# Kernel optimization log

Hardware: AMD Instinct MI355X
Metric: run time of the kernel (lower is better)

Reference implementation:

```python
import jax, jax.numpy as jnp
import numpy as np

EPS = 1e-5
K = 20

def knn_idx(x, k):
    # x: (B, N, C) -> indices of k nearest neighbors (by negative squared distance, includes self)
    sq = jnp.sum(x * x, axis=-1)                                  # (B, N)
    d = 2.0 * jnp.einsum('bnc,bmc->bnm', x, x) - sq[:, :, None] - sq[:, None, :]
    return jax.lax.top_k(d, k)[1]                                 # (B, N, k)

def edge_conv(x, k, W, g, b, rm, rv):
    # x: (B, N, C); W: (O, 2C); BN params: (O,). Returns (B, N, O).
    idx = knn_idx(x, k)
    feat = jax.vmap(lambda xt, i: xt[i])(x, idx)                  # (B, N, k, C) neighbor gather
    ctr = jnp.broadcast_to(x[:, :, None, :], feat.shape)
    edge = jnp.concatenate([feat - ctr, ctr], axis=-1)            # (B, N, k, 2C)
    h = jnp.einsum('bnkc,oc->bnko', edge, W)                      # 1x1 conv
    h = g * (h - rm) * jax.lax.rsqrt(rv + EPS) + b                # BN (eval, running stats)
    h = jnp.where(h > 0, h, 0.2 * h)                              # LeakyReLU(0.2)
    return jnp.max(h, axis=2)                                     # max over k

def bn(h, g, b, rm, rv):
    return g * (h - rm) * jax.lax.rsqrt(rv + EPS) + b

def lrelu(h):
    return jnp.where(h > 0, h, 0.2 * h)

def _bn_params(key, c):
    k1, k2 = jax.random.split(key)
    g = 1.0 + 0.1 * jax.random.normal(k1, (c,), dtype=jnp.float32)
    b = 0.1 * jax.random.normal(k2, (c,), dtype=jnp.float32)
    return g, b, jnp.zeros((c,), jnp.float32), jnp.ones((c,), jnp.float32)

def setup_inputs() -> dict:
    key = jax.random.key(0)
    ks = jax.random.split(key, 16)
    B, Cin, N = 8, 6, 4096
    d = {'x': jax.random.normal(ks[0], (B, Cin, N), dtype=jnp.float32)}
    def w(k, o, i):
        return jax.random.normal(k, (o, i), dtype=jnp.float32) * (1.0 / np.sqrt(i))
    d['W1'] = w(ks[1], 64, 12);   d['g1'], d['b1'], d['m1'], d['v1'] = _bn_params(ks[2], 64)
    d['W2'] = w(ks[3], 64, 128);  d['g2'], d['b2'], d['m2'], d['v2'] = _bn_params(ks[4], 64)
    d['W3'] = w(ks[5], 128, 128); d['g3'], d['b3'], d['m3'], d['v3'] = _bn_params(ks[6], 128)
    d['W4'] = w(ks[7], 256, 256); d['g4'], d['b4'], d['m4'], d['v4'] = _bn_params(ks[8], 256)
    d['W5'] = w(ks[9], 1024, 512); d['g5'], d['b5'], d['m5'], d['v5'] = _bn_params(ks[10], 1024)
    d['L1'] = w(ks[11], 512, 2048); d['gl1'], d['bl1'], d['ml1'], d['vl1'] = _bn_params(ks[12], 512)
    d['L2'] = w(ks[13], 256, 512); d['L2b'] = jnp.zeros((256,), jnp.float32)
    d['gl2'], d['bl2'], d['ml2'], d['vl2'] = _bn_params(ks[14], 256)
    d['L3'] = w(ks[15], 2, 256);  d['L3b'] = jnp.zeros((2,), jnp.float32)
    return d

def reference(x, W1, g1, b1, m1, v1, W2, g2, b2, m2, v2, W3, g3, b3, m3, v3,
              W4, g4, b4, m4, v4, W5, g5, b5, m5, v5,
              L1, gl1, bl1, ml1, vl1, L2, L2b, gl2, bl2, ml2, vl2, L3, L3b):
    xt = jnp.transpose(x, (0, 2, 1))                              # (B, N, 6)
    x1 = edge_conv(xt, K, W1, g1, b1, m1, v1)                     # (B, N, 64)
    x2 = edge_conv(x1, K, W2, g2, b2, m2, v2)                     # (B, N, 64)
    x3 = edge_conv(x2, K, W3, g3, b3, m3, v3)                     # (B, N, 128)
    x4 = edge_conv(x3, K, W4, g4, b4, m4, v4)                     # (B, N, 256)
    xc = jnp.concatenate([x1, x2, x3, x4], axis=-1)               # (B, N, 512)
    h = lrelu(bn(jnp.einsum('bnc,oc->bno', xc, W5), g5, b5, m5, v5))  # (B, N, 1024)
    pooled = jnp.concatenate([jnp.max(h, axis=1), jnp.mean(h, axis=1)], axis=-1)  # (B, 2048)
    o = lrelu(bn(pooled @ L1.T, gl1, bl1, ml1, vl1))
    o = lrelu(bn(o @ L2.T + L2b, gl2, bl2, ml2, vl2))
    return o @ L3.T + L3b                                         # (B, 2)
```

## Files before the change

kernel.cpp:

```cpp
#include <hip/hip_runtime.h>


#define NPTS   4096
#define NB     8
#define BNR    32768
#define KNN    20
#define EPSBN  1e-5f

__device__ __forceinline__ float lrelu(float x){ return x > 0.f ? x : 0.2f*x; }

__global__ __launch_bounds__(256) void k_transpose_pad(const float* __restrict__ x,
                                                       float* __restrict__ xt){
  int id = blockIdx.x*256 + threadIdx.x;
  int b = id >> 12, n = id & (NPTS-1);
  const float* xb = x + (size_t)b*6*NPTS + n;
  float* o = xt + (size_t)id*8;
#pragma unroll
  for (int c = 0; c < 6; ++c) o[c] = xb[(size_t)c*NPTS];
  o[6] = 0.f; o[7] = 0.f;
}

__global__ __launch_bounds__(256) void k_sqnorm(const float* __restrict__ X, int xstride, int c4,
                                                float* __restrict__ sq){
  int id = blockIdx.x*256 + threadIdx.x;
  const float4* r = (const float4*)(X + (size_t)id*xstride);
  float s = 0.f;
  for (int c = 0; c < c4; ++c){ float4 v = r[c]; s += v.x*v.x + v.y*v.y + v.z*v.z + v.w*v.w; }
  sq[id] = s;
}

__global__ __launch_bounds__(256) void k_dgemm(const float* __restrict__ X, int xstride, int Kdim,
                                               const float* __restrict__ sqv,
                                               float* __restrict__ D){
  const int bi = blockIdx.y, bj = blockIdx.x;
  if (bj < bi) return;
  __shared__ float As[16][132];
  __shared__ float Bs[16][132];
  const int i0 = bi*128, j0 = bj*128;
  const int tid = threadIdx.x, tx = tid & 15, ty = tid >> 4;
  float acc[8][8] = {};
  for (int k0 = 0; k0 < Kdim; k0 += 16){
#pragma unroll
    for (int i = 0; i < 8; ++i){
      int li = tid + 256*i;
      int row = li >> 4, kk = li & 15;
      bool ok = (k0 + kk) < Kdim;
      As[kk][row] = ok ? X[(size_t)(i0+row)*xstride + k0+kk] : 0.f;
      Bs[kk][row] = ok ? X[(size_t)(j0+row)*xstride + k0+kk] : 0.f;
    }
    __syncthreads();
#pragma unroll
    for (int kk = 0; kk < 16; ++kk){
      float a[8], b[8];
      *(float4*)&a[0] = *(const float4*)&As[kk][ty*8];
      *(float4*)&a[4] = *(const float4*)&As[kk][ty*8+4];
      *(float4*)&b[0] = *(const float4*)&Bs[kk][tx*4];
      *(float4*)&b[4] = *(const float4*)&Bs[kk][64 + tx*4];
#pragma unroll
      for (int r = 0; r < 8; ++r)
#pragma unroll
        for (int c = 0; c < 8; ++c)
          acc[r][c] = fmaf(a[r], b[c], acc[r][c]);
    }
    __syncthreads();
  }
  float sj[8];
#pragma unroll
  for (int c = 0; c < 4; ++c){
    sj[c]   = sqv[j0 + tx*4 + c];
    sj[c+4] = sqv[j0 + 64 + tx*4 + c];
  }
  float si[8];
#pragma unroll
  for (int r = 0; r < 8; ++r) si[r] = sqv[i0 + ty*8 + r];
#pragma unroll
  for (int r = 0; r < 8; ++r)
#pragma unroll
    for (int c = 0; c < 8; ++c)
      acc[r][c] = 2.f*acc[r][c] - si[r] - sj[c];
#pragma unroll
  for (int r = 0; r < 8; ++r){
    float* drow = D + (size_t)(i0 + ty*8 + r)*NPTS;
    *(float4*)&drow[j0 + tx*4]      = make_float4(acc[r][0], acc[r][1], acc[r][2], acc[r][3]);
    *(float4*)&drow[j0 + 64 + tx*4] = make_float4(acc[r][4], acc[r][5], acc[r][6], acc[r][7]);
  }
  if (bj > bi){
#pragma unroll
    for (int c = 0; c < 4; ++c){
      float* drow0 = D + (size_t)(j0 + tx*4 + c)*NPTS + i0 + ty*8;
      *(float4*)&drow0[0] = make_float4(acc[0][c], acc[1][c], acc[2][c], acc[3][c]);
      *(float4*)&drow0[4] = make_float4(acc[4][c], acc[5][c], acc[6][c], acc[7][c]);
      float* drow1 = D + (size_t)(j0 + 64 + tx*4 + c)*NPTS + i0 + ty*8;
      *(float4*)&drow1[0] = make_float4(acc[0][c+4], acc[1][c+4], acc[2][c+4], acc[3][c+4]);
      *(float4*)&drow1[4] = make_float4(acc[4][c+4], acc[5][c+4], acc[6][c+4], acc[7][c+4]);
    }
  }
}

__global__ __launch_bounds__(256) void k_scan(const float* __restrict__ D,
                                              int* __restrict__ idx){
  const int lane = threadIdx.x & 63;
  const int wv   = threadIdx.x >> 6;
  const int row  = blockIdx.x*4 + wv;
  const float* drow = D + (size_t)row*NPTS;
  float bv = -1e30f; int bi = -1;
  float thr = -1e30f;
  float dcur = drow[lane];
  for (int m0 = 0; m0 < NPTS; m0 += 64){
    float dnext = (m0 + 64 < NPTS) ? drow[m0 + 64 + lane] : -1e30f;
    unsigned long long mask = __ballot(dcur > thr);
    while (mask){
      int l = __ffsll(mask) - 1;
      mask &= mask - 1;
      float dv = __shfl(dcur, l);
      if (dv > thr){
        float upv = __shfl_up(bv, 1);
        int   upi = __shfl_up(bi, 1);
        if (lane < KNN){
          bool ins  = dv > bv;
          bool insp = (lane > 0) && (dv > upv);
          if (ins){ bv = insp ? upv : dv; bi = insp ? upi : (m0 + l); }
        }
        thr = __shfl(bv, KNN-1);
      }
    }
    dcur = dnext;
  }
  if (lane < KNN) idx[(size_t)row*KNN + lane] = bi;
}

__global__ __launch_bounds__(256) void k_gemm_xw(const float* __restrict__ X, int xstride, int Kdim,
                                                 const float* __restrict__ W, int wstride,
                                                 float* __restrict__ Out, int ostride){
  __shared__ float Xs[16][68];
  __shared__ float Ws[16][68];
  const int m0 = blockIdx.x*64, o0 = blockIdx.y*64;
  const int tid = threadIdx.x, tx = tid & 15, ty = tid >> 4;
  float acc[4][4] = {};
  for (int k0 = 0; k0 < Kdim; k0 += 16){
#pragma unroll
    for (int i = 0; i < 4; ++i){
      int li = tid + 256*i;
      int row = li >> 4, kk = li & 15;
      bool ok = (k0 + kk) < Kdim;
      Xs[kk][row] = ok ? X[(size_t)(m0+row)*xstride + k0+kk] : 0.f;
      Ws[kk][row] = ok ? W[(size_t)(o0+row)*wstride + k0+kk] : 0.f;
    }
    __syncthreads();
#pragma unroll
    for (int kk = 0; kk < 16; ++kk){
      float xa[4], wb[4];
      *(float4*)xa = *(const float4*)&Xs[kk][ty*4];
      *(float4*)wb = *(const float4*)&Ws[kk][tx*4];
#pragma unroll
      for (int i = 0; i < 4; ++i)
#pragma unroll
        for (int j = 0; j < 4; ++j)
          acc[i][j] = fmaf(xa[i], wb[j], acc[i][j]);
    }
    __syncthreads();
  }
#pragma unroll
  for (int i = 0; i < 4; ++i){
    float4 v = make_float4(acc[i][0], acc[i][1], acc[i][2], acc[i][3]);
    *(float4*)&Out[(size_t)(m0+ty*4+i)*ostride + o0 + tx*4] = v;
  }
}

__global__ __launch_bounds__(256) void k_gather_conv(const float* __restrict__ P,
                                                     const float* __restrict__ Q,
                                                     const int* __restrict__ idx,
                                                     const float* __restrict__ g,
                                                     const float* __restrict__ bb,
                                                     const float* __restrict__ rm,
                                                     const float* __restrict__ rv,
                                                     float* __restrict__ Out, int oshift, int choff){
  const int O = 1 << oshift;
  int id = blockIdx.x*256 + threadIdx.x;
  int gn = id >> oshift;
  int o  = id & (O-1);
  int bbase = (gn >> 12) * NPTS;
  const int* ip = idx + (size_t)gn*KNN;
  float vmax = -1e30f, vmin = 1e30f;
#pragma unroll
  for (int k = 0; k < KNN; ++k){
    int m = ip[k];
    float v = P[((size_t)(bbase + m) << oshift) + o];
    vmax = fmaxf(vmax, v);
    vmin = fminf(vmin, v);
  }
  float scale = g[o] * rsqrtf(rv[o] + EPSBN);
  float beta  = bb[o] - rm[o]*scale;
  float R = (scale >= 0.f) ? vmax : vmin;
  float h = R - P[((size_t)gn << oshift) + o] + Q[((size_t)gn << oshift) + o];
  Out[(size_t)gn*512 + choff + o] = lrelu(fmaf(scale, h, beta));
}

__global__ __launch_bounds__(256) void k_gemm_w5_pool(const float* __restrict__ X,
                                                      const float* __restrict__ W,
                                                      const float* __restrict__ g,
                                                      const float* __restrict__ bb,
                                                      const float* __restrict__ rm,
                                                      const float* __restrict__ rv,
                                                      float* __restrict__ pmax,
                                                      float* __restrict__ psum){
  __shared__ float Xs[16][132];
  __shared__ float Ws[16][132];
  __shared__ float red[2][16][128];
  const int m0 = blockIdx.x*128, o0 = blockIdx.y*128;
  const int tid = threadIdx.x, tx = tid & 15, ty = tid >> 4;
  float acc[8][8] = {};
  for (int k0 = 0; k0 < 512; k0 += 16){
#pragma unroll
    for (int i = 0; i < 8; ++i){
      int li = tid + 256*i;
      int row = li >> 4, kk = li & 15;
      Xs[kk][row] = X[(size_t)(m0+row)*512 + k0+kk];
      Ws[kk][row] = W[(size_t)(o0+row)*512 + k0+kk];
    }
    __syncthreads();
#pragma unroll
    for (int kk = 0; kk < 16; ++kk){
      float xa[8], wb[8];
      *(float4*)&xa[0] = *(const float4*)&Xs[kk][ty*8];
      *(float4*)&xa[4] = *(const float4*)&Xs[kk][ty*8+4];
      *(float4*)&wb[0] = *(const float4*)&Ws[kk][tx*4];
      *(float4*)&wb[4] = *(const float4*)&Ws[kk][64 + tx*4];
#pragma unroll
      for (int i = 0; i < 8; ++i)
#pragma unroll
        for (int j = 0; j < 8; ++j)
          acc[i][j] = fmaf(xa[i], wb[j], acc[i][j]);
    }
    __syncthreads();
  }
#pragma unroll
  for (int j = 0; j < 8; ++j){
    int ocol = (j < 4) ? (tx*4 + j) : (64 + tx*4 + j - 4);
    int o = o0 + ocol;
    float scale = g[o] * rsqrtf(rv[o] + EPSBN);
    float beta  = bb[o] - rm[o]*scale;
    float mx = -1e30f, sm = 0.f;
#pragma unroll
    for (int i = 0; i < 8; ++i){
      float h = lrelu(fmaf(scale, acc[i][j], beta));
      mx = fmaxf(mx, h);
      sm += h;
    }
    red[0][ty][ocol] = mx;
    red[1][ty][ocol] = sm;
  }
  __syncthreads();
  if (tid < 128){
    float mx = -1e30f, sm = 0.f;
#pragma unroll
    for (int t = 0; t < 16; ++t){
      mx = fmaxf(mx, red[0][t][tid]);
      sm += red[1][t][tid];
    }
    pmax[(size_t)blockIdx.x*1024 + o0 + tid] = mx;
    psum[(size_t)blockIdx.x*1024 + o0 + tid] = sm;
  }
}

__global__ __launch_bounds__(256) void k_pool_reduce(const float* __restrict__ pmax,
                                                     const float* __restrict__ psum,
                                                     float* __restrict__ pooled){
  int id = blockIdx.x*256 + threadIdx.x;
  int b = id >> 10, o = id & 1023;
  float mx = -1e30f, sm = 0.f;
  for (int t = 0; t < 32; ++t){
    mx = fmaxf(mx, pmax[(size_t)(b*32+t)*1024 + o]);
    sm += psum[(size_t)(b*32+t)*1024 + o];
  }
  pooled[(size_t)b*2048 + o] = mx;
  pooled[(size_t)b*2048 + 1024 + o] = sm * (1.f/NPTS);
}

__global__ __launch_bounds__(256) void k_fc1(const float* __restrict__ pooled,
                                             const float* __restrict__ W,
                                             const float* __restrict__ g,
                                             const float* __restrict__ bb,
                                             const float* __restrict__ rm,
                                             const float* __restrict__ rv,
                                             float* __restrict__ out){
  __shared__ float4 xs[512];
  int b = blockIdx.x >> 1;
  int o = ((blockIdx.x & 1) << 8) + threadIdx.x;
  const float4* pr = (const float4*)(pooled + (size_t)b*2048);
  for (int l = threadIdx.x; l < 512; l += 256) xs[l] = pr[l];
  __syncthreads();
  const float4* wr = (const float4*)(W + (size_t)o*2048);
  float s0=0.f, s1=0.f, s2=0.f, s3=0.f;
#pragma unroll 4
  for (int c = 0; c < 512; ++c){
    float4 w = wr[c], v = xs[c];
    s0 = fmaf(v.x, w.x, s0); s1 = fmaf(v.y, w.y, s1);
    s2 = fmaf(v.z, w.z, s2); s3 = fmaf(v.w, w.w, s3);
  }
  float h = (s0+s1)+(s2+s3);
  float scale = g[o] * rsqrtf(rv[o] + EPSBN);
  float beta  = bb[o] - rm[o]*scale;
  out[(size_t)b*512 + o] = lrelu(fmaf(scale, h, beta));
}

__global__ __launch_bounds__(256) void k_fc2(const float* __restrict__ in,
                                             const float* __restrict__ W,
                                             const float* __restrict__ bias,
                                             const float* __restrict__ g,
                                             const float* __restrict__ bb,
                                             const float* __restrict__ rm,
                                             const float* __restrict__ rv,
                                             float* __restrict__ out){
  __shared__ float4 xs[128];
  int b = blockIdx.x;
  int o = threadIdx.x;
  const float4* pr = (const float4*)(in + (size_t)b*512);
  if (threadIdx.x < 128) xs[threadIdx.x] = pr[threadIdx.x];
  __syncthreads();
  const float4* wr = (const float4*)(W + (size_t)o*512);
  float s0=0.f, s1=0.f, s2=0.f, s3=0.f;
#pragma unroll 4
  for (int c = 0; c < 128; ++c){
    float4 w = wr[c], v = xs[c];
    s0 = fmaf(v.x, w.x, s0); s1 = fmaf(v.y, w.y, s1);
    s2 = fmaf(v.z, w.z, s2); s3 = fmaf(v.w, w.w, s3);
  }
  float h = (s0+s1)+(s2+s3) + bias[o];
  float scale = g[o] * rsqrtf(rv[o] + EPSBN);
  float beta  = bb[o] - rm[o]*scale;
  out[(size_t)b*256 + o] = lrelu(fmaf(scale, h, beta));
}

__global__ __launch_bounds__(64) void k_fc3(const float* __restrict__ in,
                                            const float* __restrict__ W,
                                            const float* __restrict__ bias,
                                            float* __restrict__ out){
  int t = threadIdx.x;
  if (t >= 16) return;
  int b = t >> 1, o = t & 1;
  const float* xr = in + (size_t)b*256;
  const float* wr = W + (size_t)o*256;
  float s = 0.f;
  for (int c = 0; c < 256; ++c) s = fmaf(xr[c], wr[c], s);
  out[b*2 + o] = s + bias[o];
}

extern "C" void kernel_launch(void* const* d_in, const int* in_sizes, int n_in,
                              void* d_out, int out_size, void* d_ws, size_t ws_size,
                              hipStream_t stream){
  (void)in_sizes; (void)n_in; (void)out_size;
  const float* x   = (const float*)d_in[0];
  const float* W1  = (const float*)d_in[1];
  const float* g1  = (const float*)d_in[2];
  const float* b1  = (const float*)d_in[3];
  const float* m1  = (const float*)d_in[4];
  const float* v1  = (const float*)d_in[5];
  const float* W2  = (const float*)d_in[6];
  const float* g2  = (const float*)d_in[7];
  const float* b2  = (const float*)d_in[8];
  const float* m2  = (const float*)d_in[9];
  const float* v2  = (const float*)d_in[10];
  const float* W3  = (const float*)d_in[11];
  const float* g3  = (const float*)d_in[12];
  const float* b3  = (const float*)d_in[13];
  const float* m3  = (const float*)d_in[14];
  const float* v3  = (const float*)d_in[15];
  const float* W4  = (const float*)d_in[16];
  const float* g4  = (const float*)d_in[17];
  const float* b4  = (const float*)d_in[18];
  const float* m4  = (const float*)d_in[19];
  const float* v4  = (const float*)d_in[20];
  const float* W5  = (const float*)d_in[21];
  const float* g5  = (const float*)d_in[22];
  const float* b5  = (const float*)d_in[23];
  const float* m5  = (const float*)d_in[24];
  const float* v5  = (const float*)d_in[25];
  const float* L1  = (const float*)d_in[26];
  const float* gl1 = (const float*)d_in[27];
  const float* bl1 = (const float*)d_in[28];
  const float* ml1 = (const float*)d_in[29];
  const float* vl1 = (const float*)d_in[30];
  const float* L2  = (const float*)d_in[31];
  const float* L2b = (const float*)d_in[32];
  const float* gl2 = (const float*)d_in[33];
  const float* bl2 = (const float*)d_in[34];
  const float* vl2_g = (const float*)d_in[36];
  const float* ml2 = (const float*)d_in[35];
  const float* L3  = (const float*)d_in[37];
  const float* L3b = (const float*)d_in[38];

  float* ws   = (float*)d_ws;
  float* xt   = ws;
  float* sq   = ws + 262144;
  int*   idx  = (int*)(ws + 294912);
  float* Dbuf = ws + 950272;
  float* P    = Dbuf;
  float* Q    = Dbuf + 8388608;
  float* xc   = ws + 17727488;
  float* pmax = ws + 34504704;
  float* psum = ws + 34766848;
  float* pool = ws + 35028992;
  float* oA   = ws + 35045376;
  float* oB   = ws + 35049472;
  if (ws_size < (size_t)35051520 * 4) return;

  k_transpose_pad<<<128, 256, 0, stream>>>(x, xt);

  k_sqnorm<<<128, 256, 0, stream>>>(xt, 8, 2, sq);
  for (int b = 0; b < NB; ++b){
    k_dgemm<<<dim3(32,32), 256, 0, stream>>>(xt + (size_t)b*NPTS*8, 8, 8, sq + b*NPTS, Dbuf);
    k_scan<<<1024, 256, 0, stream>>>(Dbuf, idx + (size_t)b*NPTS*KNN);
  }
  k_gemm_xw<<<dim3(512,1), 256, 0, stream>>>(xt, 8, 6, W1,     12, P, 64);
  k_gemm_xw<<<dim3(512,1), 256, 0, stream>>>(xt, 8, 6, W1 + 6, 12, Q, 64);
  k_gather_conv<<<8192, 256, 0, stream>>>(P, Q, idx, g1, b1, m1, v1, xc, 6, 0);

  k_sqnorm<<<128, 256, 0, stream>>>(xc, 512, 16, sq);
  for (int b = 0; b < NB; ++b){
    k_dgemm<<<dim3(32,32), 256, 0, stream>>>(xc + (size_t)b*NPTS*512, 512, 64, sq + b*NPTS, Dbuf);
    k_scan<<<1024, 256, 0, stream>>>(Dbuf, idx + (size_t)b*NPTS*KNN);
  }
  k_gemm_xw<<<dim3(512,1), 256, 0, stream>>>(xc, 512, 64, W2,      128, P, 64);
  k_gemm_xw<<<dim3(512,1), 256, 0, stream>>>(xc, 512, 64, W2 + 64, 128, Q, 64);
  k_gather_conv<<<8192, 256, 0, stream>>>(P, Q, idx, g2, b2, m2, v2, xc, 6, 64);

  k_sqnorm<<<128, 256, 0, stream>>>(xc + 64, 512, 16, sq);
  for (int b = 0; b < NB; ++b){
    k_dgemm<<<dim3(32,32), 256, 0, stream>>>(xc + 64 + (size_t)b*NPTS*512, 512, 64, sq + b*NPTS, Dbuf);
    k_scan<<<1024, 256, 0, stream>>>(Dbuf, idx + (size_t)b*NPTS*KNN);
  }
  k_gemm_xw<<<dim3(512,2), 256, 0, stream>>>(xc + 64, 512, 64, W3,      128, P, 128);
  k_gemm_xw<<<dim3(512,2), 256, 0, stream>>>(xc + 64, 512, 64, W3 + 64, 128, Q, 128);
  k_gather_conv<<<16384, 256, 0, stream>>>(P, Q, idx, g3, b3, m3, v3, xc, 7, 128);

  k_sqnorm<<<128, 256, 0, stream>>>(xc + 128, 512, 32, sq);
  for (int b = 0; b < NB; ++b){
    k_dgemm<<<dim3(32,32), 256, 0, stream>>>(xc + 128 + (size_t)b*NPTS*512, 512, 128, sq + b*NPTS, Dbuf);
    k_scan<<<1024, 256, 0, stream>>>(Dbuf, idx + (size_t)b*NPTS*KNN);
  }
  k_gemm_xw<<<dim3(512,4), 256, 0, stream>>>(xc + 128, 512, 128, W4,       256, P, 256);
  k_gemm_xw<<<dim3(512,4), 256, 0, stream>>>(xc + 128, 512, 128, W4 + 128, 256, Q, 256);
  k_gather_conv<<<32768, 256, 0, stream>>>(P, Q, idx, g4, b4, m4, v4, xc, 8, 256);

  k_gemm_w5_pool<<<dim3(256,8), 256, 0, stream>>>(xc, W5, g5, b5, m5, v5, pmax, psum);
  k_pool_reduce<<<32, 256, 0, stream>>>(pmax, psum, pool);

  k_fc1<<<16, 256, 0, stream>>>(pool, L1, gl1, bl1, ml1, vl1, oA);
  k_fc2<<<8, 256, 0, stream>>>(oA, L2, L2b, gl2, bl2, ml2, vl2_g, oB);
  k_fc3<<<1, 64, 0, stream>>>(oB, L3, L3b, (float*)d_out);
}
```

Baseline: 3.577 ms.

## Fuse distance GEMM with top-k selection and merge P/Q projection GEMMs

Replaces the per-batch distance-matrix GEMM plus separate wavefront scan with one fused kernel. Each block computes 64 rows of distances against 128-column tiles and keeps a running top-20 in shared memory, filtering candidates by a per-row threshold through a small capped candidate buffer. This removes the 64MB distance-matrix write and read per batch and the 16 serial launches per layer. It also merges the two projection GEMMs into one kernel writing an interleaved PQ buffer. The trade-off is a serial single-thread-per-row insertion sort and extra block barriers inside the column loop, and the grid is only 512 blocks.

```diff
diff --git a/kernel.cpp b/kernel.cpp
--- a/kernel.cpp
+++ b/kernel.cpp
@@ -6,6 +6,7 @@
 #define BNR    32768
 #define KNN    20
 #define EPSBN  1e-5f
+#define CAP    12
 
 __device__ __forceinline__ float lrelu(float x){ return x > 0.f ? x : 0.2f*x; }
 
@@ -29,131 +30,160 @@
   sq[id] = s;
 }
 
-__global__ __launch_bounds__(256) void k_dgemm(const float* __restrict__ X, int xstride, int Kdim,
-                                               const float* __restrict__ sqv,
-                                               float* __restrict__ D){
-  const int bi = blockIdx.y, bj = blockIdx.x;
-  if (bj < bi) return;
-  __shared__ float As[16][132];
-  __shared__ float Bs[16][132];
-  const int i0 = bi*128, j0 = bj*128;
+template<int K>
+__global__ __launch_bounds__(256) void k_knn_fused(const float* __restrict__ X, int xstride,
+                                                   const float* __restrict__ sqv,
+                                                   int* __restrict__ idx){
+  constexpr int BK = (K < 32) ? K : 32;
+  __shared__ float As[BK][68];
+  __shared__ float Bs[BK][132];
+  __shared__ float sqs[128];
+  __shared__ float thr[64];
+  __shared__ float lv[64][KNN];
+  __shared__ int   li[64][KNN];
+  __shared__ int   cnt[64];
+  __shared__ float cv[64][CAP];
+  __shared__ int   ci[64][CAP];
+
+  const int b  = blockIdx.y;
+  const int i0 = blockIdx.x * 64;
   const int tid = threadIdx.x, tx = tid & 15, ty = tid >> 4;
-  float acc[8][8] = {};
+  const float* Xb  = X + (size_t)b * NPTS * xstride;
+  const float* sqb = sqv + b * NPTS;
+
+  if (tid < 64){
+    thr[tid] = -3e38f; cnt[tid] = 0;
+#pragma unroll
+    for (int j = 0; j < KNN; ++j){ lv[tid][j] = -3e38f; li[tid][j] = 0; }
+  }
+  float sqi[4];
+#pragma unroll
+  for (int r = 0; r < 4; ++r) sqi[r] = sqb[i0 + ty*4 + r];
+
+  for (int j0 = 0; j0 < NPTS; j0 += 128){
+    float acc[4][8] = {};
+    for (int k0 = 0; k0 < K; k0 += BK){
+      {
+        int row = tid & 63, q = tid >> 6;
+        const float* src = Xb + (size_t)(i0 + row)*xstride + k0;
+#pragma unroll
+        for (int k = q*(BK/4); k < (q+1)*(BK/4); ++k) As[k][row] = src[k];
+      }
+      {
+        int col = tid & 127, h = tid >> 7;
+        const float* src = Xb + (size_t)(j0 + col)*xstride + k0;
+#pragma unroll
+        for (int k = h*(BK/2); k < (h+1)*(BK/2); ++k) Bs[k][col] = src[k];
+      }
+      if (k0 == 0 && tid < 128) sqs[tid] = sqb[j0 + tid];
+      __syncthreads();
+#pragma unroll
+      for (int kk = 0; kk < BK; ++kk){
+        float a[4], bb_[8];
+        *(float4*)a        = *(const float4*)&As[kk][ty*4];
+        *(float4*)&bb_[0]  = *(const float4*)&Bs[kk][tx*4];
+        *(float4*)&bb_[4]  = *(const float4*)&Bs[kk][64 + tx*4];
+#pragma unroll
+        for (int r = 0; r < 4; ++r)
+#pragma unroll
+          for (int c = 0; c < 8; ++c)
+            acc[r][c] = fmaf(a[r], bb_[c], acc[r][c]);
+      }
+      __syncthreads();
+    }
+    float sq8[8];
+#pragma unroll
+    for (int c = 0; c < 4; ++c){ sq8[c] = sqs[tx*4 + c]; sq8[c+4] = sqs[64 + tx*4 + c]; }
+
+    unsigned pending = 0xFFFFFFFFu;
+    while (true){
+      if (pending){
+        float tr[4];
+#pragma unroll
+        for (int r = 0; r < 4; ++r) tr[r] = thr[ty*4 + r];
+#pragma unroll
+        for (int r = 0; r < 4; ++r)
+#pragma unroll
+          for (int c = 0; c < 8; ++c){
+            unsigned bit = 1u << (r*8 + c);
+            if (pending & bit){
+              float val = 2.f*acc[r][c] - sqi[r] - sq8[c];
+              if (val <= tr[r]) pending &= ~bit;
+              else {
+                int row = ty*4 + r;
+                int pos = atomicAdd(&cnt[row], 1);
+                if (pos < CAP){
+                  int col = (c < 4) ? (j0 + tx*4 + c) : (j0 + 64 + tx*4 + c - 4);
+                  cv[row][pos] = val; ci[row][pos] = col;
+                  pending &= ~bit;
+                }
+              }
+            }
+          }
+      }
+      int any = __syncthreads_or(pending != 0u);
+      if (tid < 64){
+        int n = min(cnt[tid], CAP);
+        for (int i2 = 0; i2 < n; ++i2){
+          float val = cv[tid][i2]; int cc = ci[tid][i2];
+          if (val > lv[tid][KNN-1]){
+            int j = KNN-1;
+            while (j > 0 && lv[tid][j-1] < val){
+              lv[tid][j] = lv[tid][j-1]; li[tid][j] = li[tid][j-1]; --j;
+            }
+            lv[tid][j] = val; li[tid][j] = cc;
+          }
+        }
+        thr[tid] = lv[tid][KNN-1];
+        cnt[tid] = 0;
+      }
+      __syncthreads();
+      if (!any) break;
+    }
+  }
+  if (tid < 64){
+    int gn = b*NPTS + i0 + tid;
+#pragma unroll
+    for (int j = 0; j < KNN; ++j) idx[(size_t)gn*KNN + j] = li[tid][j];
+  }
+}
+
+__global__ __launch_bounds__(256) void k_gemm_pq(const float* __restrict__ X, int xstride, int Kdim,
+                                                 const float* __restrict__ W, int wstride, int Och,
+                                                 float* __restrict__ PQ){
+  __shared__ float Xs[16][132];
+  __shared__ float Ws[16][68];
+  const int m0 = blockIdx.x*128, o0 = blockIdx.y*64;
+  const int tid = threadIdx.x, tx = tid & 15, ty = tid >> 4;
+  const int O2 = 2*Och;
+  float acc[8][4] = {};
   for (int k0 = 0; k0 < Kdim; k0 += 16){
 #pragma unroll
     for (int i = 0; i < 8; ++i){
       int li = tid + 256*i;
       int row = li >> 4, kk = li & 15;
       bool ok = (k0 + kk) < Kdim;
-      As[kk][row] = ok ? X[(size_t)(i0+row)*xstride + k0+kk] : 0.f;
-      Bs[kk][row] = ok ? X[(size_t)(j0+row)*xstride + k0+kk] : 0.f;
-    }
-    __syncthreads();
-#pragma unroll
-    for (int kk = 0; kk < 16; ++kk){
-      float a[8], b[8];
-      *(float4*)&a[0] = *(const float4*)&As[kk][ty*8];
-      *(float4*)&a[4] = *(const float4*)&As[kk][ty*8+4];
-      *(float4*)&b[0] = *(const float4*)&Bs[kk][tx*4];
-      *(float4*)&b[4] = *(const float4*)&Bs[kk][64 + tx*4];
-#pragma unroll
-      for (int r = 0; r < 8; ++r)
-#pragma unroll
-        for (int c = 0; c < 8; ++c)
-          acc[r][c] = fmaf(a[r], b[c], acc[r][c]);
-    }
-    __syncthreads();
-  }
-  float sj[8];
-#pragma unroll
-  for (int c = 0; c < 4; ++c){
-    sj[c]   = sqv[j0 + tx*4 + c];
-    sj[c+4] = sqv[j0 + 64 + tx*4 + c];
-  }
-  float si[8];
-#pragma unroll
-  for (int r = 0; r < 8; ++r) si[r] = sqv[i0 + ty*8 + r];
-#pragma unroll
-  for (int r = 0; r < 8; ++r)
-#pragma unroll
-    for (int c = 0; c < 8; ++c)
-      acc[r][c] = 2.f*acc[r][c] - si[r] - sj[c];
-#pragma unroll
-  for (int r = 0; r < 8; ++r){
-    float* drow = D + (size_t)(i0 + ty*8 + r)*NPTS;
-    *(float4*)&drow[j0 + tx*4]      = make_float4(acc[r][0], acc[r][1], acc[r][2], acc[r][3]);
-    *(float4*)&drow[j0 + 64 + tx*4] = make_float4(acc[r][4], acc[r][5], acc[r][6], acc[r][7]);
-  }
-  if (bj > bi){
-#pragma unroll
-    for (int c = 0; c < 4; ++c){
-      float* drow0 = D + (size_t)(j0 + tx*4 + c)*NPTS + i0 + ty*8;
-      *(float4*)&drow0[0] = make_float4(acc[0][c], acc[1][c], acc[2][c], acc[3][c]);
-      *(float4*)&drow0[4] = make_float4(acc[4][c], acc[5][c], acc[6][c], acc[7][c]);
-      float* drow1 = D + (size_t)(j0 + 64 + tx*4 + c)*NPTS + i0 + ty*8;
-      *(float4*)&drow1[0] = make_float4(acc[0][c+4], acc[1][c+4], acc[2][c+4], acc[3][c+4]);
-      *(float4*)&drow1[4] = make_float4(acc[4][c+4], acc[5][c+4], acc[6][c+4], acc[7][c+4]);
-    }
-  }
-}
-
-__global__ __launch_bounds__(256) void k_scan(const float* __restrict__ D,
-                                              int* __restrict__ idx){
-  const int lane = threadIdx.x & 63;
-  const int wv   = threadIdx.x >> 6;
-  const int row  = blockIdx.x*4 + wv;
-  const float* drow = D + (size_t)row*NPTS;
-  float bv = -1e30f; int bi = -1;
-  float thr = -1e30f;
-  float dcur = drow[lane];
-  for (int m0 = 0; m0 < NPTS; m0 += 64){
-    float dnext = (m0 + 64 < NPTS) ? drow[m0 + 64 + lane] : -1e30f;
-    unsigned long long mask = __ballot(dcur > thr);
-    while (mask){
-      int l = __ffsll(mask) - 1;
-      mask &= mask - 1;
-      float dv = __shfl(dcur, l);
-      if (dv > thr){
-        float upv = __shfl_up(bv, 1);
-        int   upi = __shfl_up(bi, 1);
-        if (lane < KNN){
-          bool ins  = dv > bv;
-          bool insp = (lane > 0) && (dv > upv);
-          if (ins){ bv = insp ? upv : dv; bi = insp ? upi : (m0 + l); }
-        }
-        thr = __shfl(bv, KNN-1);
-      }
-    }
-    dcur = dnext;
-  }
-  if (lane < KNN) idx[(size_t)row*KNN + lane] = bi;
-}
-
-__global__ __launch_bounds__(256) void k_gemm_xw(const float* __restrict__ X, int xstride, int Kdim,
-                                                 const float* __restrict__ W, int wstride,
-                                                 float* __restrict__ Out, int ostride){
-  __shared__ float Xs[16][68];
-  __shared__ float Ws[16][68];
-  const int m0 = blockIdx.x*64, o0 = blockIdx.y*64;
-  const int tid = threadIdx.x, tx = tid & 15, ty = tid >> 4;
-  float acc[4][4] = {};
-  for (int k0 = 0; k0 < Kdim; k0 += 16){
+      Xs[kk][row] = ok ? X[(size_t)(m0+row)*xstride + k0+kk] : 0.f;
+    }
 #pragma unroll
     for (int i = 0; i < 4; ++i){
       int li = tid + 256*i;
       int row = li >> 4, kk = li & 15;
+      int orow = o0 + row;
+      const float* wr = (orow < Och) ? (W + (size_t)orow*wstride)
+                                     : (W + (size_t)(orow-Och)*wstride + Kdim);
       bool ok = (k0 + kk) < Kdim;
-      Xs[kk][row] = ok ? X[(size_t)(m0+row)*xstride + k0+kk] : 0.f;
-      Ws[kk][row] = ok ? W[(size_t)(o0+row)*wstride + k0+kk] : 0.f;
+      Ws[kk][row] = ok ? wr[k0+kk] : 0.f;
     }
     __syncthreads();
 #pragma unroll
     for (int kk = 0; kk < 16; ++kk){
-      float xa[4], wb[4];
-      *(float4*)xa = *(const float4*)&Xs[kk][ty*4];
-      *(float4*)wb = *(const float4*)&Ws[kk][tx*4];
-#pragma unroll
-      for (int i = 0; i < 4; ++i)
+      float xa[8], wb[4];
+      *(float4*)&xa[0] = *(const float4*)&Xs[kk][ty*8];
+      *(float4*)&xa[4] = *(const float4*)&Xs[kk][ty*8+4];
+      *(float4*)wb     = *(const float4*)&Ws[kk][tx*4];
+#pragma unroll
+      for (int i = 0; i < 8; ++i)
 #pragma unroll
         for (int j = 0; j < 4; ++j)
           acc[i][j] = fmaf(xa[i], wb[j], acc[i][j]);
@@ -161,14 +191,13 @@
     __syncthreads();
   }
 #pragma unroll
-  for (int i = 0; i < 4; ++i){
+  for (int i = 0; i < 8; ++i){
     float4 v = make_float4(acc[i][0], acc[i][1], acc[i][2], acc[i][3]);
-    *(float4*)&Out[(size_t)(m0+ty*4+i)*ostride + o0 + tx*4] = v;
-  }
-}
-
-__global__ __launch_bounds__(256) void k_gather_conv(const float* __restrict__ P,
-                                                     const float* __restrict__ Q,
+    *(float4*)&PQ[(size_t)(m0+ty*8+i)*O2 + o0 + tx*4] = v;
+  }
+}
+
+__global__ __launch_bounds__(256) void k_gather_conv(const float* __restrict__ PQ,
                                                      const int* __restrict__ idx,
                                                      const float* __restrict__ g,
                                                      const float* __restrict__ bb,
@@ -181,18 +210,19 @@
   int o  = id & (O-1);
   int bbase = (gn >> 12) * NPTS;
   const int* ip = idx + (size_t)gn*KNN;
-  float vmax = -1e30f, vmin = 1e30f;
+  float vmax = -3e38f, vmin = 3e38f;
 #pragma unroll
   for (int k = 0; k < KNN; ++k){
     int m = ip[k];
-    float v = P[((size_t)(bbase + m) << oshift) + o];
+    float v = PQ[((size_t)(bbase + m) << (oshift+1)) + o];
     vmax = fmaxf(vmax, v);
     vmin = fminf(vmin, v);
   }
   float scale = g[o] * rsqrtf(rv[o] + EPSBN);
   float beta  = bb[o] - rm[o]*scale;
   float R = (scale >= 0.f) ? vmax : vmin;
-  float h = R - P[((size_t)gn << oshift) + o] + Q[((size_t)gn << oshift) + o];
+  size_t self = (size_t)gn << (oshift+1);
+  float h = R - PQ[self + o] + PQ[self + O + o];
   Out[(size_t)gn*512 + choff + o] = lrelu(fmaf(scale, h, beta));
 }
 
@@ -240,7 +270,7 @@
     int o = o0 + ocol;
     float scale = g[o] * rsqrtf(rv[o] + EPSBN);
     float beta  = bb[o] - rm[o]*scale;
-    float mx = -1e30f, sm = 0.f;
+    float mx = -3e38f, sm = 0.f;
 #pragma unroll
     for (int i = 0; i < 8; ++i){
       float h = lrelu(fmaf(scale, acc[i][j], beta));
@@ -252,7 +282,7 @@
   }
   __syncthreads();
   if (tid < 128){
-    float mx = -1e30f, sm = 0.f;
+    float mx = -3e38f, sm = 0.f;
 #pragma unroll
     for (int t = 0; t < 16; ++t){
       mx = fmaxf(mx, red[0][t][tid]);
@@ -268,7 +298,7 @@
                                                      float* __restrict__ pooled){
   int id = blockIdx.x*256 + threadIdx.x;
   int b = id >> 10, o = id & 1023;
-  float mx = -1e30f, sm = 0.f;
+  float mx = -3e38f, sm = 0.f;
   for (int t = 0; t < 32; ++t){
     mx = fmaxf(mx, pmax[(size_t)(b*32+t)*1024 + o]);
     sm += psum[(size_t)(b*32+t)*1024 + o];
@@ -385,8 +415,8 @@
   const float* L2b = (const float*)d_in[32];
   const float* gl2 = (const float*)d_in[33];
   const float* bl2 = (const float*)d_in[34];
-  const float* vl2_g = (const float*)d_in[36];
   const float* ml2 = (const float*)d_in[35];
+  const float* vl2 = (const float*)d_in[36];
   const float* L3  = (const float*)d_in[37];
   const float* L3b = (const float*)d_in[38];
 
@@ -394,9 +424,7 @@
   float* xt   = ws;
   float* sq   = ws + 262144;
   int*   idx  = (int*)(ws + 294912);
-  float* Dbuf = ws + 950272;
-  float* P    = Dbuf;
-  float* Q    = Dbuf + 8388608;
+  float* PQ   = ws + 950272;
   float* xc   = ws + 17727488;
   float* pmax = ws + 34504704;
   float* psum = ws + 34766848;
@@ -408,45 +436,29 @@
   k_transpose_pad<<<128, 256, 0, stream>>>(x, xt);
 
   k_sqnorm<<<128, 256, 0, stream>>>(xt, 8, 2, sq);
-  for (int b = 0; b < NB; ++b){
-    k_dgemm<<<dim3(32,32), 256, 0, stream>>>(xt + (size_t)b*NPTS*8, 8, 8, sq + b*NPTS, Dbuf);
-    k_scan<<<1024, 256, 0, stream>>>(Dbuf, idx + (size_t)b*NPTS*KNN);
-  }
-  k_gemm_xw<<<dim3(512,1), 256, 0, stream>>>(xt, 8, 6, W1,     12, P, 64);
-  k_gemm_xw<<<dim3(512,1), 256, 0, stream>>>(xt, 8, 6, W1 + 6, 12, Q, 64);
-  k_gather_conv<<<8192, 256, 0, stream>>>(P, Q, idx, g1, b1, m1, v1, xc, 6, 0);
+  k_knn_fused<8><<<dim3(64,8), 256, 0, stream>>>(xt, 8, sq, idx);
+  k_gemm_pq<<<dim3(256,2), 256, 0, stream>>>(xt, 8, 6, W1, 12, 64, PQ);
+  k_gather_conv<<<8192, 256, 0, stream>>>(PQ, idx, g1, b1, m1, v1, xc, 6, 0);
 
   k_sqnorm<<<128, 256, 0, stream>>>(xc, 512, 16, sq);
-  for (int b = 0; b < NB; ++b){
-    k_dgemm<<<dim3(32,32), 256, 0, stream>>>(xc + (size_t)b*NPTS*512, 512, 64, sq + b*NPTS, Dbuf);
-    k_scan<<<1024, 256, 0, stream>>>(Dbuf, idx + (size_t)b*NPTS*KNN);
-  }
-  k_gemm_xw<<<dim3(512,1), 256, 0, stream>>>(xc, 512, 64, W2,      128, P, 64);
-  k_gemm_xw<<<dim3(512,1), 256, 0, stream>>>(xc, 512, 64, W2 + 64, 128, Q, 64);
-  k_gather_conv<<<8192, 256, 0, stream>>>(P, Q, idx, g2, b2, m2, v2, xc, 6, 64);
+  k_knn_fused<64><<<dim3(64,8), 256, 0, stream>>>(xc, 512, sq, idx);
+  k_gemm_pq<<<dim3(256,2), 256, 0, stream>>>(xc, 512, 64, W2, 128, 64, PQ);
+  k_gather_conv<<<8192, 256, 0, stream>>>(PQ, idx, g2, b2, m2, v2, xc, 6, 64);
 
   k_sqnorm<<<128, 256, 0, stream>>>(xc + 64, 512, 16, sq);
-  for (int b = 0; b < NB; ++b){
-    k_dgemm<<<dim3(32,32), 256, 0, stream>>>(xc + 64 + (size_t)b*NPTS*512, 512, 64, sq + b*NPTS, Dbuf);
-    k_scan<<<1024, 256, 0, stream>>>(Dbuf, idx + (size_t)b*NPTS*KNN);
-  }
-  k_gemm_xw<<<dim3(512,2), 256, 0, stream>>>(xc + 64, 512, 64, W3,      128, P, 128);
-  k_gemm_xw<<<dim3(512,2), 256, 0, stream>>>(xc + 64, 512, 64, W3 + 64, 128, Q, 128);
-  k_gather_conv<<<16384, 256, 0, stream>>>(P, Q, idx, g3, b3, m3, v3, xc, 7, 128);
+  k_knn_fused<64><<<dim3(64,8), 256, 0, stream>>>(xc + 64, 512, sq, idx);
+  k_gemm_pq<<<dim3(256,4), 256, 0, stream>>>(xc + 64, 512, 64, W3, 128, 128, PQ);
+  k_gather_conv<<<16384, 256, 0, stream>>>(PQ, idx, g3, b3, m3, v3, xc, 7, 128);
 
   k_sqnorm<<<128, 256, 0, stream>>>(xc + 128, 512, 32, sq);
-  for (int b = 0; b < NB; ++b){
-    k_dgemm<<<dim3(32,32), 256, 0, stream>>>(xc + 128 + (size_t)b*NPTS*512, 512, 128, sq + b*NPTS, Dbuf);
-    k_scan<<<1024, 256, 0, stream>>>(Dbuf, idx + (size_t)b*NPTS*KNN);
-  }
-  k_gemm_xw<<<dim3(512,4), 256, 0, stream>>>(xc + 128, 512, 128, W4,       256, P, 256);
-  k_gemm_xw<<<dim3(512,4), 256, 0, stream>>>(xc + 128, 512, 128, W4 + 128, 256, Q, 256);
-  k_gather_conv<<<32768, 256, 0, stream>>>(P, Q, idx, g4, b4, m4, v4, xc, 8, 256);
+  k_knn_fused<128><<<dim3(64,8), 256, 0, stream>>>(xc + 128, 512, sq, idx);
+  k_gemm_pq<<<dim3(256,8), 256, 0, stream>>>(xc + 128, 512, 128, W4, 256, 256, PQ);
+  k_gather_conv<<<32768, 256, 0, stream>>>(PQ, idx, g4, b4, m4, v4, xc, 8, 256);
 
   k_gemm_w5_pool<<<dim3(256,8), 256, 0, stream>>>(xc, W5, g5, b5, m5, v5, pmax, psum);
   k_pool_reduce<<<32, 256, 0, stream>>>(pmax, psum, pool);
 
   k_fc1<<<16, 256, 0, stream>>>(pool, L1, gl1, bl1, ml1, vl1, oA);
-  k_fc2<<<8, 256, 0, stream>>>(oA, L2, L2b, gl2, bl2, ml2, vl2_g, oB);
+  k_fc2<<<8, 256, 0, stream>>>(oA, L2, L2b, gl2, bl2, ml2, vl2, oB);
   k_fc3<<<1, 64, 0, stream>>>(oB, L3, L3b, (float*)d_out);
 }
```

New measurement: 3.325 ms. 7.0% less time.
